# Kernel tuning notes

Hardware: AMD Instinct MI355X
Metric: run time of the kernel (lower is better)

## Reference

```python
import jax, jax.numpy as jnp
import numpy as np

U, L, B = 512, 512, 256  # units, num_layers (rectangular mesh: L == U), batch
PI = float(np.pi)


def cc_mul(a, b):
    # complex multiply of stacked (real, imag) tensors
    return jnp.stack((a[0] * b[0] - a[1] * b[1], a[0] * b[1] + a[1] * b[0]))


def i_mul(c):
    # s_mul(1j, c): multiply stacked complex by 1j -> (-im, re)
    return jnp.stack((-c[1], c[0]))


def setup_inputs() -> dict:
    key = jax.random.key(0)
    ks = jax.random.split(key, 8)
    x = jax.random.normal(ks[0], (2, B, U), jnp.float32)
    two_pi = 2.0 * PI
    theta = jax.random.uniform(ks[1], (L, U // 2), jnp.float32) * two_pi
    phi = jax.random.uniform(ks[2], (L, U // 2), jnp.float32) * two_pi
    gamma = jax.random.uniform(ks[3], (U,), jnp.float32) * two_pi
    mask = jnp.ones((L, U // 2), jnp.float32)
    enn = jax.random.uniform(ks[4], (U, L), jnp.float32)
    enp = jax.random.uniform(ks[5], (U, L), jnp.float32)
    epn = jax.random.uniform(ks[6], (U, L), jnp.float32)
    epp = jax.random.uniform(ks[7], (U, L), jnp.float32)
    # rectangular-mesh permutations: identity at input/output, interior layers
    # alternate circular shifts so MZIs couple (0,1),(2,3),... then (1,2),(3,4),...
    perms = np.tile(np.arange(U, dtype=np.int32), (L + 1, 1))
    for l in range(1, L):
        perms[l] = np.roll(perms[l], 1 if l % 2 else -1)
    perms = jnp.asarray(perms)
    # pairwise off-diagonal permutation: swap adjacent pairs [1,0,3,2,...]
    pairwise_perm = jnp.asarray(
        np.arange(U, dtype=np.int32).reshape(-1, 2)[:, ::-1].ravel())
    return dict(x=x, theta=theta, phi=phi, gamma=gamma, mask=mask,
                enn=enn, enp=enp, epn=epn, epp=epp,
                perms=perms, pairwise_perm=pairwise_perm)


def reference(x, theta, phi, gamma, mask, enn, enp, epn, epp, perms, pairwise_perm):
    # --- MeshPhasesTorch (basis='sm', hadamard=False) ---
    inv = 1.0 - mask
    th = theta * mask + inv * PI  # (1 - hadamard) * pi
    ph = phi * mask + inv * PI

    def stripe(p):  # single_mode_arrangement: [L, U//2] -> [U, L]
        return jnp.zeros((U, L), p.dtype).at[::2].set(p.T)

    internal = stripe(th)
    external = stripe(ph)
    ipsl = jnp.stack((jnp.cos(internal), jnp.sin(internal)))  # [2, U, L]
    epsl = jnp.stack((jnp.cos(external), jnp.sin(external)))  # [2, U, L]

    roll_m1 = lambda t: jnp.roll(t, -1, axis=1)  # along units axis
    roll_p1 = lambda t: jnp.roll(t, 1, axis=1)

    # --- MeshTorch.mesh_layers (hadamard=False branch) ---
    s11 = epp * ipsl - enn * roll_m1(ipsl)
    s22 = roll_p1(-enn * ipsl + epp * roll_m1(ipsl))
    s12 = i_mul(roll_p1(enp * ipsl + epn * roll_m1(ipsl)))
    s21 = i_mul(epn * ipsl + enp * roll_m1(ipsl))

    diag = cc_mul(epsl, s11 + s22) * 0.5              # [2, U, L]
    off = cc_mul(roll_p1(epsl), s21 + s12) * 0.5      # [2, U, L]
    diag = jnp.transpose(diag, (0, 2, 1))             # [2, L, U]
    off = jnp.transpose(off, (0, 2, 1))

    # --- forward: input phase shift, then sequential vertical layers ---
    in_ps = jnp.stack((jnp.cos(gamma), jnp.sin(gamma)))  # [2, U]
    out = cc_mul(x, in_ps[:, None, :])                   # [2, B, U]
    out = out[..., perms[0]]                             # left perm of layer 0

    def step(carry, inp):
        d, o, rp = inp  # [2, U], [2, U], [U]
        y = cc_mul(carry, d[:, None, :]) \
            + cc_mul(carry, o[:, None, :])[..., pairwise_perm]
        return y[..., rp], None

    xs = (jnp.moveaxis(diag, 1, 0), jnp.moveaxis(off, 1, 0), perms[1:])
    out, _ = jax.lax.scan(step, out, xs)
    return out
```

## Files before the change

### kernel.cpp

```cpp
#include <hip/hip_runtime.h>
#include <hip/hip_fp16.h>


#define UU 512
#define LL 512
#define BB 256
#define KK 256
#define KF 4
#define N9 128
#define W9 9
#define N17 64
#define W17 17
#define N33 32
#define W33 33


__global__ __launch_bounds__(512, 2) void mesh_build4(
    const float* __restrict__ theta, const float* __restrict__ phi,
    const float* __restrict__ enn,   const float* __restrict__ enp,
    const float* __restrict__ epn,   const float* __restrict__ epp,
    float2* __restrict__ g9)
{
    __shared__ float2 gwj[7 * UU];
    __shared__ float2 xbuf[2][UU];
    const int u  = threadIdx.x;
    const int j  = ((blockIdx.x & 7) << 4) | (blockIdx.x >> 3);
    const int um = (u + UU - 1) & (UU - 1);
    const int l0 = j * KF;

    const float4 epp_u4 = *(const float4*)(epp + u * LL + l0);
    const float4 epp_m4 = *(const float4*)(epp + um * LL + l0);
    const float4 enn_u4 = *(const float4*)(enn + u * LL + l0);
    const float4 enn_m4 = *(const float4*)(enn + um * LL + l0);
    const float4 enp_u4 = *(const float4*)(enp + u * LL + l0);
    const float4 enp_m4 = *(const float4*)(enp + um * LL + l0);
    const float4 epn_u4 = *(const float4*)(epn + u * LL + l0);
    const float4 epn_m4 = *(const float4*)(epn + um * LL + l0);
    const float epp_u8[4] = {epp_u4.x, epp_u4.y, epp_u4.z, epp_u4.w};
    const float epp_m8[4] = {epp_m4.x, epp_m4.y, epp_m4.z, epp_m4.w};
    const float enn_u8[4] = {enn_u4.x, enn_u4.y, enn_u4.z, enn_u4.w};
    const float enn_m8[4] = {enn_m4.x, enn_m4.y, enn_m4.z, enn_m4.w};
    const float enp_u8[4] = {enp_u4.x, enp_u4.y, enp_u4.z, enp_u4.w};
    const float enp_m8[4] = {enp_m4.x, enp_m4.y, enp_m4.z, enp_m4.w};
    const float epn_u8[4] = {epn_u4.x, epn_u4.y, epn_u4.z, epn_u4.w};
    const float epn_m8[4] = {epn_m4.x, epn_m4.y, epn_m4.z, epn_m4.w};

    const int ka = u >> 1;
    const int kb = ((u + 1) >> 1) & (KK - 1);
    float thA[KF], thB[KF], phC[KF];
    #pragma unroll
    for (int s = 0; s < KF; ++s) {
        thA[s] = theta[(l0 + s) * KK + ka];
        thB[s] = theta[(l0 + s) * KK + kb];
        phC[s] = phi  [(l0 + s) * KK + ka];
    }

    const bool uodd = (u & 1) != 0;

    #define COEF(s, DR, DI, OR_, OI_) { \
        float sA, cA, sB, cB, sC, cC; \
        __sincosf(thA[s], &sA, &cA); \
        __sincosf(thB[s], &sB, &cB); \
        __sincosf(phC[s], &sC, &cC); \
        const float ipu_r = uodd ? 1.f : cA, ipu_i = uodd ? 0.f : sA; \
        const float ipp_r = uodd ? cB : 1.f, ipp_i = uodd ? sB : 0.f; \
        const float ipm_r = uodd ? cA : 1.f, ipm_i = uodd ? sA : 0.f; \
        const float epu_r = uodd ? 1.f : cC, epu_i = uodd ? 0.f : sC; \
        const float epm_r = uodd ? cC : 1.f, epm_i = uodd ? sC : 0.f; \
        const float sd_r = epp_u8[s]*ipu_r - enn_u8[s]*ipp_r - enn_m8[s]*ipm_r + epp_m8[s]*ipu_r; \
        const float sd_i = epp_u8[s]*ipu_i - enn_u8[s]*ipp_i - enn_m8[s]*ipm_i + epp_m8[s]*ipu_i; \
        DR = 0.5f * (epu_r * sd_r - epu_i * sd_i); \
        DI = 0.5f * (epu_r * sd_i + epu_i * sd_r); \
        const float so_r = epn_u8[s]*ipu_r + enp_u8[s]*ipp_r + enp_m8[s]*ipm_r + epn_m8[s]*ipu_r; \
        const float so_i = epn_u8[s]*ipu_i + enp_u8[s]*ipp_i + enp_m8[s]*ipm_i + epn_m8[s]*ipu_i; \
        const float soi_r = -so_i, soi_i = so_r; \
        OR_ = 0.5f * (epm_r * soi_r - epm_i * soi_i); \
        OI_ = 0.5f * (epm_r * soi_i + epm_i * soi_r); }

    float dcur_r, dcur_i, o0_r, o0_i;
    COEF(0, dcur_r, dcur_i, o0_r, o0_i)
    gwj[u] = make_float2(1.f, 0.f);
    xbuf[0][u] = make_float2(o0_r, o0_i);
    __syncthreads();

    int sigma = 0;
    const int tb = uodd ? 0 : 2;
    float2 outr[W9];

    #pragma unroll
    for (int s = 0; s < KF; ++s) {
        const int W  = 2 * s + 1;
        const int Wn = W + 2;
        const int a  = (u + sigma) & (UU - 1);
        const int bx = ((u ^ 1) + sigma) & (UU - 1);
        const float2 ox = xbuf[s & 1][u ^ 1];
        const float dr = dcur_r, di = dcur_i, orr = ox.x, oi = ox.y;

        #pragma unroll
        for (int tn = 0; tn < W9; ++tn) {
            float ar = 0.f, ai = 0.f;
            if (tn < Wn) {
                const int tp = tn - 1;
                const int ts = tn - tb;
                if (0 <= tp && tp < W) {
                    float2 gv = gwj[tp * UU + a];
                    ar += dr * gv.x - di * gv.y;
                    ai += dr * gv.y + di * gv.x;
                }
                if (0 <= ts && ts < W) {
                    float2 gv = gwj[ts * UU + bx];
                    ar += orr * gv.x - oi * gv.y;
                    ai += orr * gv.y + oi * gv.x;
                }
            }
            outr[tn] = make_float2(ar, ai);
        }

        if (s < KF - 1) {
            float dn_r, dn_i, on_r, on_i;
            COEF(s + 1, dn_r, dn_i, on_r, on_i)
            __syncthreads();
            const int wd = (u + sigma) & (UU - 1);
            #pragma unroll
            for (int tn = 0; tn < W9; ++tn)
                if (tn < Wn) gwj[tn * UU + wd] = outr[tn];
            xbuf[(s + 1) & 1][u] = make_float2(on_r, on_i);
            dcur_r = dn_r; dcur_i = dn_i;
            sigma += (s & 1) ? 1 : -1;
            __syncthreads();
        }
    }
    #undef COEF

    const int v = (j == N9 - 1) ? u : um;
    #pragma unroll
    for (int t = 0; t < W9; ++t)
        g9[(j * W9 + t) * UU + v] = outr[t];
}

__global__ __launch_bounds__(512, 2) void mesh_merge_both(
    const float2* __restrict__ g9, __half2* __restrict__ g2h)
{
    __shared__ float2 lds1[W17 * UU];
    const int u = threadIdx.x;
    const int q = blockIdx.x;

    {
        const int jA = 4 * q + 1, jB = 4 * q;
        float2 a[W9];
        #pragma unroll
        for (int ta = 0; ta < W9; ++ta)
            a[ta] = g9[(jA * W9 + ta) * UU + u];

        float2 outv[W17];
        #pragma unroll
        for (int t = 0; t < W17; ++t) outv[t] = make_float2(0.f, 0.f);

        #pragma unroll
        for (int ta = 0; ta < W9; ++ta) {
            const int k = (u - 4 + ta + UU) & (UU - 1);
            float2 brow[W9];
            #pragma unroll
            for (int tbq = 0; tbq < W9; ++tbq)
                brow[tbq] = g9[(jB * W9 + tbq) * UU + k];
            #pragma unroll
            for (int tbq = 0; tbq < W9; ++tbq) {
                outv[ta + tbq].x += a[ta].x * brow[tbq].x - a[ta].y * brow[tbq].y;
                outv[ta + tbq].y += a[ta].x * brow[tbq].y + a[ta].y * brow[tbq].x;
            }
        }
        #pragma unroll
        for (int t = 0; t < W17; ++t) lds1[t * UU + u] = outv[t];
    }

    float2 r2[W17];
    {
        const int jA = 4 * q + 3, jB = 4 * q + 2;
        const int loA = (jA == N9 - 1) ? -5 : -4;
        float2 a[W9];
        #pragma unroll
        for (int ta = 0; ta < W9; ++ta)
            a[ta] = g9[(jA * W9 + ta) * UU + u];

        #pragma unroll
        for (int t = 0; t < W17; ++t) r2[t] = make_float2(0.f, 0.f);

        #pragma unroll
        for (int ta = 0; ta < W9; ++ta) {
            const int k = (u + loA + ta + UU) & (UU - 1);
            float2 brow[W9];
            #pragma unroll
            for (int tbq = 0; tbq < W9; ++tbq)
                brow[tbq] = g9[(jB * W9 + tbq) * UU + k];
            #pragma unroll
            for (int tbq = 0; tbq < W9; ++tbq) {
                r2[ta + tbq].x += a[ta].x * brow[tbq].x - a[ta].y * brow[tbq].y;
                r2[ta + tbq].y += a[ta].x * brow[tbq].y + a[ta].y * brow[tbq].x;
            }
        }
    }
    __syncthreads();

    {
        const int loC = (q == N33 - 1) ? -9 : -8;
        float2 outv[W33];
        #pragma unroll
        for (int t = 0; t < W33; ++t) outv[t] = make_float2(0.f, 0.f);

        #pragma unroll
        for (int ta = 0; ta < W17; ++ta) {
            const int k = (u + loC + ta + UU) & (UU - 1);
            #pragma unroll
            for (int tbq = 0; tbq < W17; ++tbq) {
                const float2 bv = lds1[tbq * UU + k];
                outv[ta + tbq].x += r2[ta].x * bv.x - r2[ta].y * bv.y;
                outv[ta + tbq].y += r2[ta].x * bv.y + r2[ta].y * bv.x;
            }
        }
        #pragma unroll
        for (int t = 0; t < W33; ++t)
            g2h[(q * W33 + t) * UU + u] = __floats2half2_rn(outv[t].x, outv[t].y);
    }
}

__global__ __launch_bounds__(512, 2) void mesh_apply(
    const float* __restrict__ x, const float* __restrict__ gamma,
    const __half2* __restrict__ g2h, float* __restrict__ out)
{
    __shared__ float2 sbuf[2][548];
    const int u = threadIdx.x;
    const int b = blockIdx.x;

    float sg, cg;
    __sincosf(gamma[u], &sg, &cg);
    const float xr = x[b * UU + u];
    const float xi = x[BB * UU + b * UU + u];
    float2 v = make_float2(xr * cg - xi * sg, xr * sg + xi * cg);

    #define STORE_STATE(pp)                                                   \
        do {                                                                  \
            sbuf[pp][u + 17] = v;                                             \
            if (u >= 495) sbuf[pp][u - 495] = v;          \
            if (u < 16)   sbuf[pp][u + 529] = v;          \
        } while (0)

    STORE_STATE(0);

    float2 gg[W33];
    {
        const __half2* gq = g2h + u;
        #pragma unroll
        for (int t = 0; t < W33; ++t) gg[t] = __half22float2(gq[t * UU]);
    }
    __syncthreads();

    for (int q = 0; q < N33; ++q) {
        const int p = q & 1;
        const int base = u + ((q == N33 - 1) ? 0 : 1);

        float2 w[W33];
        #pragma unroll
        for (int t = 0; t < W33; ++t) w[t] = sbuf[p][base + t];

        float ar = 0.f, ai = 0.f;
        #pragma unroll
        for (int t = 0; t < W33; ++t) {
            ar += gg[t].x * w[t].x - gg[t].y * w[t].y;
            ai += gg[t].x * w[t].y + gg[t].y * w[t].x;
        }
        v = make_float2(ar, ai);

        if (q < N33 - 1) {
            const __half2* gq = g2h + (q + 1) * (W33 * UU) + u;
            #pragma unroll
            for (int t = 0; t < W33; ++t) gg[t] = __half22float2(gq[t * UU]);
            STORE_STATE(1 - p);
            __syncthreads();
        }
    }

    out[b * UU + u]           = v.x;
    out[BB * UU + b * UU + u] = v.y;
    #undef STORE_STATE
}

#define RSLOTS 6
#define WAITVM40() __builtin_amdgcn_s_waitcnt(0x8F78)
#define STAGE(gg, ss)                                                        \
    _Pragma("unroll")                                                        \
    for (int jq = 0; jq < 8; ++jq)                                           \
        __builtin_amdgcn_global_load_lds(                                    \
            (const __attribute__((address_space(1))) void*)(coef + (gg) * UU + jq * 64 + lane), \
            (__attribute__((address_space(3))) void*)&ring[(ss) * UU + jq * 64], \
            16, 0, 0);

__global__ __launch_bounds__(512) void mesh_precompute_slot(
    const float* __restrict__ theta, const float* __restrict__ phi,
    const float* __restrict__ enn,   const float* __restrict__ enp,
    const float* __restrict__ epn,   const float* __restrict__ epp,
    float4* __restrict__ coef)
{
    const int u  = threadIdx.x;
    const int l  = blockIdx.x;
    const int um = (u + UU - 1) & (UU - 1);
    const float epp_u  = epp[u * LL + l],  epp_um = epp[um * LL + l];
    const float enn_u  = enn[u * LL + l],  enn_um = enn[um * LL + l];
    const float enp_u  = enp[u * LL + l],  enp_um = enp[um * LL + l];
    const float epn_u  = epn[u * LL + l],  epn_um = epn[um * LL + l];
    float ipu_r, ipu_i, ipp_r, ipp_i, ipm_r, ipm_i;
    float epu_r, epu_i, epm_r, epm_i;
    if ((u & 1) == 0) {
        const int k = u >> 1;
        float th = theta[l * KK + k];  __sincosf(th, &ipu_i, &ipu_r);
        ipp_r = 1.f; ipp_i = 0.f;  ipm_r = 1.f; ipm_i = 0.f;
        float phv = phi[l * KK + k];   __sincosf(phv, &epu_i, &epu_r);
        epm_r = 1.f; epm_i = 0.f;
    } else {
        ipu_r = 1.f; ipu_i = 0.f;
        float thp = theta[l * KK + (((u + 1) >> 1) & (KK - 1))]; __sincosf(thp, &ipp_i, &ipp_r);
        float thm = theta[l * KK + (u >> 1)];                    __sincosf(thm, &ipm_i, &ipm_r);
        epu_r = 1.f; epu_i = 0.f;
        float phm = phi[l * KK + (u >> 1)];                      __sincosf(phm, &epm_i, &epm_r);
    }
    const float sd_r = epp_u * ipu_r - enn_u * ipp_r - enn_um * ipm_r + epp_um * ipu_r;
    const float sd_i = epp_u * ipu_i - enn_u * ipp_i - enn_um * ipm_i + epp_um * ipu_i;
    const float d_r = 0.5f * (epu_r * sd_r - epu_i * sd_i);
    const float d_i = 0.5f * (epu_r * sd_i + epu_i * sd_r);
    const float so_r = epn_u * ipu_r + enp_u * ipp_r + enp_um * ipm_r + epn_um * ipu_r;
    const float so_i = epn_u * ipu_i + enp_u * ipp_i + enp_um * ipm_i + epn_um * ipu_i;
    const float soi_r = -so_i, soi_i = so_r;
    const float o_r = 0.5f * (epm_r * soi_r - epm_i * soi_i);
    const float o_i = 0.5f * (epm_r * soi_i + epm_i * soi_r);
    const int slot = ((u & 7) << 6) | (u >> 3);
    coef[l * UU + slot] = make_float4(d_r, d_i, o_r, o_i);
}

#define PAIR_MIX(K)                                                         \
    _Pragma("unroll")                                                       \
    for (int p = 0; p < 4; ++p) {                                           \
        const float4 ke = K[2*p], ko = K[2*p+1];                            \
        y0r[p] = c0r[p]*ke.x - c0i[p]*ke.y + c1r[p]*ko.z - c1i[p]*ko.w;     \
        y0i[p] = c0r[p]*ke.y + c0i[p]*ke.x + c1r[p]*ko.w + c1i[p]*ko.z;     \
        y1r[p] = c1r[p]*ko.x - c1i[p]*ko.y + c0r[p]*ke.z - c0i[p]*ke.w;     \
        y1i[p] = c1r[p]*ko.y + c1i[p]*ko.x + c0r[p]*ke.w + c0i[p]*ke.z;     \
    }

__global__ __launch_bounds__(64) void mesh_chain_r3(
    const float* __restrict__ x, const float* __restrict__ gamma,
    const float4* __restrict__ coef, float* __restrict__ out)
{
    __shared__ float4 ring[RSLOTS * UU];
    const int lane = threadIdx.x;
    const int b    = blockIdx.x;
    const int m0   = lane << 3;
    #pragma unroll
    for (int pl = 0; pl < RSLOTS; ++pl) { STAGE(pl, pl) }
    const float4 xr0 = *(const float4*)(x + b * UU + m0);
    const float4 xr1 = *(const float4*)(x + b * UU + m0 + 4);
    const float4 xi0 = *(const float4*)(x + BB * UU + b * UU + m0);
    const float4 xi1 = *(const float4*)(x + BB * UU + b * UU + m0 + 4);
    const float xr[8] = {xr0.x, xr0.y, xr0.z, xr0.w, xr1.x, xr1.y, xr1.z, xr1.w};
    const float xi[8] = {xi0.x, xi0.y, xi0.z, xi0.w, xi1.x, xi1.y, xi1.z, xi1.w};
    float c0r[4], c0i[4], c1r[4], c1i[4];
    #pragma unroll
    for (int p = 0; p < 4; ++p) {
        float s0, cg0, s1, cg1;
        __sincosf(gamma[m0 + 2*p],     &s0, &cg0);
        __sincosf(gamma[m0 + 2*p + 1], &s1, &cg1);
        c0r[p] = xr[2*p] * cg0 - xi[2*p] * s0;
        c0i[p] = xr[2*p] * s0  + xi[2*p] * cg0;
        c1r[p] = xr[2*p+1] * cg1 - xi[2*p+1] * s1;
        c1i[p] = xr[2*p+1] * s1  + xi[2*p+1] * cg1;
    }
    const int laneM1 = (lane + 63) & 63;
    const int laneP1 = (lane + 1) & 63;
    int sa = 0;
    for (int it = 0; it < 256; ++it) {
        float y0r[4], y0i[4], y1r[4], y1i[4];
        WAITVM40();
        float4 k[8];
        #pragma unroll
        for (int q = 0; q < 8; ++q) k[q] = ring[sa * UU + q * 64 + lane];
        PAIR_MIX(k)
        {
            const float br = __shfl(y1r[3], laneM1, 64);
            const float bi = __shfl(y1i[3], laneM1, 64);
            #pragma unroll
            for (int p = 3; p > 0; --p) { c0r[p] = y1r[p-1]; c0i[p] = y1i[p-1]; }
            c0r[0] = br; c0i[0] = bi;
            #pragma unroll
            for (int p = 0; p < 4; ++p) { c1r[p] = y0r[p]; c1i[p] = y0i[p]; }
        }
        { const int g1 = (2 * it + RSLOTS) & (LL - 1); STAGE(g1, sa) }
        WAITVM40();
        float4 n[8];
        #pragma unroll
        for (int q = 0; q < 8; ++q) n[q] = ring[(sa + 1) * UU + q * 64 + lane];
        PAIR_MIX(n)
        if (it < 255) {
            const float br = __shfl(y0r[0], laneP1, 64);
            const float bi = __shfl(y0i[0], laneP1, 64);
            #pragma unroll
            for (int p = 0; p < 3; ++p) { c0r[p] = y1r[p]; c0i[p] = y1i[p];
                                          c1r[p] = y0r[p+1]; c1i[p] = y0i[p+1]; }
            c0r[3] = y1r[3]; c0i[3] = y1i[3];
            c1r[3] = br;     c1i[3] = bi;
        } else {
            #pragma unroll
            for (int p = 0; p < 4; ++p) { c0r[p] = y0r[p]; c0i[p] = y0i[p];
                                          c1r[p] = y1r[p]; c1i[p] = y1i[p]; }
        }
        { const int g2 = (2 * it + RSLOTS + 1) & (LL - 1); STAGE(g2, sa + 1) }
        sa += 2; if (sa >= RSLOTS) sa = 0;
    }
    *(float4*)(out + b * UU + m0)               = make_float4(c0r[0], c1r[0], c0r[1], c1r[1]);
    *(float4*)(out + b * UU + m0 + 4)           = make_float4(c0r[2], c1r[2], c0r[3], c1r[3]);
    *(float4*)(out + BB * UU + b * UU + m0)     = make_float4(c0i[0], c1i[0], c0i[1], c1i[1]);
    *(float4*)(out + BB * UU + b * UU + m0 + 4) = make_float4(c0i[2], c1i[2], c0i[3], c1i[3]);
}

extern "C" void kernel_launch(void* const* d_in, const int* in_sizes, int n_in,
                              void* d_out, int out_size, void* d_ws, size_t ws_size,
                              hipStream_t stream) {
    (void)in_sizes; (void)n_in; (void)out_size;
    const float* x     = (const float*)d_in[0];
    const float* theta = (const float*)d_in[1];
    const float* phi   = (const float*)d_in[2];
    const float* gamma = (const float*)d_in[3];
    const float* enn   = (const float*)d_in[5];
    const float* enp   = (const float*)d_in[6];
    const float* epn   = (const float*)d_in[7];
    const float* epp   = (const float*)d_in[8];
    float* out = (float*)d_out;

    if (ws_size >= (size_t)6881280) {
        float2*  g9  = (float2*)d_ws;
        __half2* g2h = (__half2*)((char*)d_ws + 4718592);

        mesh_build4<<<N9, UU, 0, stream>>>(theta, phi, enn, enp, epn, epp, g9);
        mesh_merge_both<<<N33, UU, 0, stream>>>(g9, g2h);
        mesh_apply<<<BB, UU, 0, stream>>>(x, gamma, g2h, out);
    } else {
        float4* coef = (float4*)d_ws;
        mesh_precompute_slot<<<LL, UU, 0, stream>>>(theta, phi, enn, enp, epn, epp, coef);
        mesh_chain_r3<<<BB, 64, 0, stream>>>(x, gamma, coef, out);
    }
}
```

Measured before the change: 151.0 us.

## Fuse band build and merge kernels, keeping per-block bands in LDS

Merges the band-building kernel and the merge kernel into one kernel with 32 blocks. Each block builds its four 9-wide bands one after another into shared memory and then runs both merge levels from shared memory. This removes one kernel launch and the global-memory round trip of the fp32 intermediate bands, and shrinks the workspace. In exchange, build parallelism drops from 128 blocks to 32, each block does four builds in series, and the large LDS allocation limits occupancy to one block per CU.

```diff
diff --git a/kernel.cpp b/kernel.cpp
--- a/kernel.cpp
+++ b/kernel.cpp
@@ -15,47 +15,20 @@
 #define W33 33
 
 
-__global__ __launch_bounds__(512, 2) void mesh_build4(
+__global__ __launch_bounds__(512, 2) void mesh_buildmerge(
     const float* __restrict__ theta, const float* __restrict__ phi,
     const float* __restrict__ enn,   const float* __restrict__ enp,
     const float* __restrict__ epn,   const float* __restrict__ epp,
-    float2* __restrict__ g9)
+    __half2* __restrict__ g2h)
 {
-    __shared__ float2 gwj[7 * UU];
+    __shared__ float2 gblk[4 * W9 * UU];
     __shared__ float2 xbuf[2][UU];
     const int u  = threadIdx.x;
-    const int j  = ((blockIdx.x & 7) << 4) | (blockIdx.x >> 3);
+    const int q  = blockIdx.x;
     const int um = (u + UU - 1) & (UU - 1);
-    const int l0 = j * KF;
-
-    const float4 epp_u4 = *(const float4*)(epp + u * LL + l0);
-    const float4 epp_m4 = *(const float4*)(epp + um * LL + l0);
-    const float4 enn_u4 = *(const float4*)(enn + u * LL + l0);
-    const float4 enn_m4 = *(const float4*)(enn + um * LL + l0);
-    const float4 enp_u4 = *(const float4*)(enp + u * LL + l0);
-    const float4 enp_m4 = *(const float4*)(enp + um * LL + l0);
-    const float4 epn_u4 = *(const float4*)(epn + u * LL + l0);
-    const float4 epn_m4 = *(const float4*)(epn + um * LL + l0);
-    const float epp_u8[4] = {epp_u4.x, epp_u4.y, epp_u4.z, epp_u4.w};
-    const float epp_m8[4] = {epp_m4.x, epp_m4.y, epp_m4.z, epp_m4.w};
-    const float enn_u8[4] = {enn_u4.x, enn_u4.y, enn_u4.z, enn_u4.w};
-    const float enn_m8[4] = {enn_m4.x, enn_m4.y, enn_m4.z, enn_m4.w};
-    const float enp_u8[4] = {enp_u4.x, enp_u4.y, enp_u4.z, enp_u4.w};
-    const float enp_m8[4] = {enp_m4.x, enp_m4.y, enp_m4.z, enp_m4.w};
-    const float epn_u8[4] = {epn_u4.x, epn_u4.y, epn_u4.z, epn_u4.w};
-    const float epn_m8[4] = {epn_m4.x, epn_m4.y, epn_m4.z, epn_m4.w};
-
+    const bool uodd = (u & 1) != 0;
     const int ka = u >> 1;
     const int kb = ((u + 1) >> 1) & (KK - 1);
-    float thA[KF], thB[KF], phC[KF];
-    #pragma unroll
-    for (int s = 0; s < KF; ++s) {
-        thA[s] = theta[(l0 + s) * KK + ka];
-        thB[s] = theta[(l0 + s) * KK + kb];
-        phC[s] = phi  [(l0 + s) * KK + ka];
-    }
-
-    const bool uodd = (u & 1) != 0;
 
     #define COEF(s, DR, DI, OR_, OI_) { \
         float sA, cA, sB, cB, sC, cC; \
@@ -77,121 +50,118 @@
         OR_ = 0.5f * (epm_r * soi_r - epm_i * soi_i); \
         OI_ = 0.5f * (epm_r * soi_i + epm_i * soi_r); }
 
-    float dcur_r, dcur_i, o0_r, o0_i;
-    COEF(0, dcur_r, dcur_i, o0_r, o0_i)
-    gwj[u] = make_float2(1.f, 0.f);
-    xbuf[0][u] = make_float2(o0_r, o0_i);
-    __syncthreads();
-
-    int sigma = 0;
-    const int tb = uodd ? 0 : 2;
-    float2 outr[W9];
-
-    #pragma unroll
-    for (int s = 0; s < KF; ++s) {
-        const int W  = 2 * s + 1;
-        const int Wn = W + 2;
-        const int a  = (u + sigma) & (UU - 1);
-        const int bx = ((u ^ 1) + sigma) & (UU - 1);
-        const float2 ox = xbuf[s & 1][u ^ 1];
-        const float dr = dcur_r, di = dcur_i, orr = ox.x, oi = ox.y;
-
-        #pragma unroll
-        for (int tn = 0; tn < W9; ++tn) {
-            float ar = 0.f, ai = 0.f;
-            if (tn < Wn) {
-                const int tp = tn - 1;
-                const int ts = tn - tb;
-                if (0 <= tp && tp < W) {
-                    float2 gv = gwj[tp * UU + a];
-                    ar += dr * gv.x - di * gv.y;
-                    ai += dr * gv.y + di * gv.x;
+    for (int sb = 0; sb < 4; ++sb) {
+        const int j  = 4 * q + sb;
+        const int l0 = j * KF;
+        float2* G = gblk + sb * (W9 * UU);
+
+        const float4 epp_u4 = *(const float4*)(epp + u * LL + l0);
+        const float4 epp_m4 = *(const float4*)(epp + um * LL + l0);
+        const float4 enn_u4 = *(const float4*)(enn + u * LL + l0);
+        const float4 enn_m4 = *(const float4*)(enn + um * LL + l0);
+        const float4 enp_u4 = *(const float4*)(enp + u * LL + l0);
+        const float4 enp_m4 = *(const float4*)(enp + um * LL + l0);
+        const float4 epn_u4 = *(const float4*)(epn + u * LL + l0);
+        const float4 epn_m4 = *(const float4*)(epn + um * LL + l0);
+        const float epp_u8[4] = {epp_u4.x, epp_u4.y, epp_u4.z, epp_u4.w};
+        const float epp_m8[4] = {epp_m4.x, epp_m4.y, epp_m4.z, epp_m4.w};
+        const float enn_u8[4] = {enn_u4.x, enn_u4.y, enn_u4.z, enn_u4.w};
+        const float enn_m8[4] = {enn_m4.x, enn_m4.y, enn_m4.z, enn_m4.w};
+        const float enp_u8[4] = {enp_u4.x, enp_u4.y, enp_u4.z, enp_u4.w};
+        const float enp_m8[4] = {enp_m4.x, enp_m4.y, enp_m4.z, enp_m4.w};
+        const float epn_u8[4] = {epn_u4.x, epn_u4.y, epn_u4.z, epn_u4.w};
+        const float epn_m8[4] = {epn_m4.x, epn_m4.y, epn_m4.z, epn_m4.w};
+
+        float thA[KF], thB[KF], phC[KF];
+        #pragma unroll
+        for (int s = 0; s < KF; ++s) {
+            thA[s] = theta[(l0 + s) * KK + ka];
+            thB[s] = theta[(l0 + s) * KK + kb];
+            phC[s] = phi  [(l0 + s) * KK + ka];
+        }
+
+        float dcur_r, dcur_i, o0_r, o0_i;
+        COEF(0, dcur_r, dcur_i, o0_r, o0_i)
+        G[u] = make_float2(1.f, 0.f);
+        xbuf[0][u] = make_float2(o0_r, o0_i);
+        __syncthreads();
+
+        int sigma = 0;
+        const int tb = uodd ? 0 : 2;
+        float2 outr[W9];
+
+        #pragma unroll
+        for (int s = 0; s < KF; ++s) {
+            const int W  = 2 * s + 1;
+            const int Wn = W + 2;
+            const int a  = (u + sigma) & (UU - 1);
+            const int bx = ((u ^ 1) + sigma) & (UU - 1);
+            const float2 ox = xbuf[s & 1][u ^ 1];
+            const float dr = dcur_r, di = dcur_i, orr = ox.x, oi = ox.y;
+
+            #pragma unroll
+            for (int tn = 0; tn < W9; ++tn) {
+                float ar = 0.f, ai = 0.f;
+                if (tn < Wn) {
+                    const int tp = tn - 1;
+                    const int ts = tn - tb;
+                    if (0 <= tp && tp < W) {
+                        float2 gv = G[tp * UU + a];
+                        ar += dr * gv.x - di * gv.y;
+                        ai += dr * gv.y + di * gv.x;
+                    }
+                    if (0 <= ts && ts < W) {
+                        float2 gv = G[ts * UU + bx];
+                        ar += orr * gv.x - oi * gv.y;
+                        ai += orr * gv.y + oi * gv.x;
+                    }
                 }
-                if (0 <= ts && ts < W) {
-                    float2 gv = gwj[ts * UU + bx];
-                    ar += orr * gv.x - oi * gv.y;
-                    ai += orr * gv.y + oi * gv.x;
-                }
+                outr[tn] = make_float2(ar, ai);
             }
-            outr[tn] = make_float2(ar, ai);
-        }
-
-        if (s < KF - 1) {
-            float dn_r, dn_i, on_r, on_i;
-            COEF(s + 1, dn_r, dn_i, on_r, on_i)
-            __syncthreads();
-            const int wd = (u + sigma) & (UU - 1);
-            #pragma unroll
-            for (int tn = 0; tn < W9; ++tn)
-                if (tn < Wn) gwj[tn * UU + wd] = outr[tn];
-            xbuf[(s + 1) & 1][u] = make_float2(on_r, on_i);
-            dcur_r = dn_r; dcur_i = dn_i;
-            sigma += (s & 1) ? 1 : -1;
-            __syncthreads();
-        }
+
+            if (s < KF - 1) {
+                float dn_r, dn_i, on_r, on_i;
+                COEF(s + 1, dn_r, dn_i, on_r, on_i)
+                __syncthreads();
+                const int wd = (u + sigma) & (UU - 1);
+                #pragma unroll
+                for (int tn = 0; tn < W9; ++tn)
+                    if (tn < Wn) G[tn * UU + wd] = outr[tn];
+                xbuf[(s + 1) & 1][u] = make_float2(on_r, on_i);
+                dcur_r = dn_r; dcur_i = dn_i;
+                sigma += (s & 1) ? 1 : -1;
+                __syncthreads();
+            }
+        }
+
+        const int v = (j == N9 - 1) ? u : um;
+        __syncthreads();
+        #pragma unroll
+        for (int t = 0; t < W9; ++t)
+            G[t * UU + v] = outr[t];
+        __syncthreads();
     }
     #undef COEF
 
-    const int v = (j == N9 - 1) ? u : um;
-    #pragma unroll
-    for (int t = 0; t < W9; ++t)
-        g9[(j * W9 + t) * UU + v] = outr[t];
-}
-
-__global__ __launch_bounds__(512, 2) void mesh_merge_both(
-    const float2* __restrict__ g9, __half2* __restrict__ g2h)
-{
-    __shared__ float2 lds1[W17 * UU];
-    const int u = threadIdx.x;
-    const int q = blockIdx.x;
-
-    {
-        const int jA = 4 * q + 1, jB = 4 * q;
-        float2 a[W9];
-        #pragma unroll
-        for (int ta = 0; ta < W9; ++ta)
-            a[ta] = g9[(jA * W9 + ta) * UU + u];
-
-        float2 outv[W17];
-        #pragma unroll
-        for (int t = 0; t < W17; ++t) outv[t] = make_float2(0.f, 0.f);
-
-        #pragma unroll
-        for (int ta = 0; ta < W9; ++ta) {
-            const int k = (u - 4 + ta + UU) & (UU - 1);
-            float2 brow[W9];
-            #pragma unroll
-            for (int tbq = 0; tbq < W9; ++tbq)
-                brow[tbq] = g9[(jB * W9 + tbq) * UU + k];
-            #pragma unroll
-            for (int tbq = 0; tbq < W9; ++tbq) {
-                outv[ta + tbq].x += a[ta].x * brow[tbq].x - a[ta].y * brow[tbq].y;
-                outv[ta + tbq].y += a[ta].x * brow[tbq].y + a[ta].y * brow[tbq].x;
-            }
-        }
-        #pragma unroll
-        for (int t = 0; t < W17; ++t) lds1[t * UU + u] = outv[t];
-    }
+    const float2* G0 = gblk + 0 * (W9 * UU);
+    const float2* G1 = gblk + 1 * (W9 * UU);
+    const float2* G2 = gblk + 2 * (W9 * UU);
+    const float2* G3 = gblk + 3 * (W9 * UU);
 
     float2 r2[W17];
     {
-        const int jA = 4 * q + 3, jB = 4 * q + 2;
-        const int loA = (jA == N9 - 1) ? -5 : -4;
+        const int loA = (4 * q + 3 == N9 - 1) ? -5 : -4;
         float2 a[W9];
         #pragma unroll
-        for (int ta = 0; ta < W9; ++ta)
-            a[ta] = g9[(jA * W9 + ta) * UU + u];
-
+        for (int ta = 0; ta < W9; ++ta) a[ta] = G3[ta * UU + u];
         #pragma unroll
         for (int t = 0; t < W17; ++t) r2[t] = make_float2(0.f, 0.f);
-
         #pragma unroll
         for (int ta = 0; ta < W9; ++ta) {
             const int k = (u + loA + ta + UU) & (UU - 1);
             float2 brow[W9];
             #pragma unroll
-            for (int tbq = 0; tbq < W9; ++tbq)
-                brow[tbq] = g9[(jB * W9 + tbq) * UU + k];
+            for (int tbq = 0; tbq < W9; ++tbq) brow[tbq] = G2[tbq * UU + k];
             #pragma unroll
             for (int tbq = 0; tbq < W9; ++tbq) {
                 r2[ta + tbq].x += a[ta].x * brow[tbq].x - a[ta].y * brow[tbq].y;
@@ -199,6 +169,32 @@
             }
         }
     }
+
+    float2 a1[W17];
+    {
+        float2 a[W9];
+        #pragma unroll
+        for (int ta = 0; ta < W9; ++ta) a[ta] = G1[ta * UU + u];
+        #pragma unroll
+        for (int t = 0; t < W17; ++t) a1[t] = make_float2(0.f, 0.f);
+        #pragma unroll
+        for (int ta = 0; ta < W9; ++ta) {
+            const int k = (u - 4 + ta + UU) & (UU - 1);
+            float2 brow[W9];
+            #pragma unroll
+            for (int tbq = 0; tbq < W9; ++tbq) brow[tbq] = G0[tbq * UU + k];
+            #pragma unroll
+            for (int tbq = 0; tbq < W9; ++tbq) {
+                a1[ta + tbq].x += a[ta].x * brow[tbq].x - a[ta].y * brow[tbq].y;
+                a1[ta + tbq].y += a[ta].x * brow[tbq].y + a[ta].y * brow[tbq].x;
+            }
+        }
+    }
+
+    float2* lds1 = gblk;
+    __syncthreads();
+    #pragma unroll
+    for (int t = 0; t < W17; ++t) lds1[t * UU + u] = a1[t];
     __syncthreads();
 
     {
@@ -206,7 +202,6 @@
         float2 outv[W33];
         #pragma unroll
         for (int t = 0; t < W33; ++t) outv[t] = make_float2(0.f, 0.f);
-
         #pragma unroll
         for (int ta = 0; ta < W17; ++ta) {
             const int k = (u + loC + ta + UU) & (UU - 1);
@@ -433,12 +428,10 @@
     const float* epp   = (const float*)d_in[8];
     float* out = (float*)d_out;
 
-    if (ws_size >= (size_t)6881280) {
-        float2*  g9  = (float2*)d_ws;
-        __half2* g2h = (__half2*)((char*)d_ws + 4718592);
-
-        mesh_build4<<<N9, UU, 0, stream>>>(theta, phi, enn, enp, epn, epp, g9);
-        mesh_merge_both<<<N33, UU, 0, stream>>>(g9, g2h);
+    if (ws_size >= (size_t)2162688) {
+        __half2* g2h = (__half2*)d_ws;
+
+        mesh_buildmerge<<<N33, UU, 0, stream>>>(theta, phi, enn, enp, epn, epp, g2h);
         mesh_apply<<<BB, UU, 0, stream>>>(x, gamma, g2h, out);
     } else {
         float4* coef = (float4*)d_ws;
```

Result: slower. 164.5 us (+9.0%).
